# Kernel tuning notes

Measured on AMD Instinct MI355X. Metric: run time of the kernel, lower is better.

## Reference

```python
import jax, jax.numpy as jnp
import numpy as np

N, H, W, C, CK, ITER = 4, 256, 256, 8, 2, 4
HID = 2 * C
C2 = C * C


def project(x, w1, b1, w2, b2, w3, b3):
    # flax Project: Dense->gelu->Dense->gelu->Dense (gelu approximate=tanh, jax default)
    h = jax.nn.gelu(x @ w1 + b1)
    h = jax.nn.gelu(h @ w2 + b2)
    return h @ w3 + b3


def setup_inputs() -> dict:
    key = jax.random.key(0)
    ks = jax.random.split(key, 40)
    d = {}
    d['u'] = jax.random.normal(ks[0], (N, H, W, C), jnp.float32)
    d['k'] = jax.random.normal(ks[1], (N, H, W, CK), jnp.float32)
    idx = 2
    # gamma MLP (in CK), delta MLP (in CK), greens real/imag MLPs (in 2)
    for nm, fin in zip(['g', 'dl', 'fr', 'fi'], [CK, CK, 2, 2]):
        for li, (fi_, fo) in enumerate([(fin, HID), (HID, HID), (HID, C2)]):
            d[f'{nm}_w{li+1}'] = jax.random.normal(ks[idx], (fi_, fo), jnp.float32) / np.sqrt(fi_).astype(np.float32)
            d[f'{nm}_b{li+1}'] = jnp.zeros((fo,), jnp.float32)
            idx += 1
    d['bias'] = jax.random.normal(ks[idx], (C,), jnp.float32)
    return d


def reference(u, k, g_w1, g_b1, g_w2, g_b2, g_w3, g_b3,
              dl_w1, dl_b1, dl_w2, dl_b2, dl_w3, dl_b3,
              fr_w1, fr_b1, fr_w2, fr_b2, fr_w3, fr_b3,
              fi_w1, fi_b1, fi_w2, fi_b2, fi_w3, fi_b3, bias):
    # per-pixel gamma / delta matrices: (N,H,W,C,C), scaled by 1/C^2 as in original
    gmat = (project(k, g_w1, g_b1, g_w2, g_b2, g_w3, g_b3) / C2).reshape(N, H, W, C, C)
    dmat = (project(k, dl_w1, dl_b1, dl_w2, dl_b2, dl_w3, dl_b3) / C2).reshape(N, H, W, C, C)
    # spectral Green's filter on the rfft grid; meshgrid(kx, ky) -> (W, H//2+1)
    kx = jnp.fft.rfftfreq(H, d=1.0 / H)
    ky = jnp.fft.fftfreq(W, d=1.0 / W)
    Kx, Ky = jnp.meshgrid(kx, ky)
    K = jnp.stack([Kx, Ky], axis=-1).astype(jnp.float32)  # (W, H//2+1, 2)
    filt_r = project(K, fr_w1, fr_b1, fr_w2, fr_b2, fr_w3, fr_b3)
    filt_i = project(K, fi_w1, fi_b1, fi_w2, fi_b2, fi_w3, fi_b3)
    filt = ((filt_r + 1j * filt_i) / C2).reshape(W, H // 2 + 1, C, C)  # H==W
    for _ in range(ITER):
        local = 2.0 * u - jnp.einsum('nhwj,nhwjk->nhwk', u, gmat)
        du = jnp.einsum('nhwj,nhwjk->nhwk', u, dmat)
        uf = jnp.fft.rfftn(du, axes=(1, 2))  # (N,H,W//2+1,C) complex
        gu = jnp.fft.irfftn(jnp.einsum('nhwj,hwjk->nhwk', uf, filt), axes=(1, 2))
        u = local + jnp.einsum('nhwj,nhwjk->nhwk', gu, gmat)
    return jax.nn.gelu(u + bias)
```

## Files before the change

kernel.cpp:

```cpp
#include <hip/hip_runtime.h>
#include <math.h>

#define NB 4
#define HB 256
#define WB 256
#define CB 8
#define NPIX (NB*HB*WB)
#define W2B 129
#define TWO_PI_F 6.283185307179586f

typedef float f32x4 __attribute__((ext_vector_type(4)));

__device__ __forceinline__ float gelu_f(float x){
    float z = 0.7978845608028654f*(x + 0.044715f*x*x*x);
    return x * __builtin_amdgcn_rcpf(1.0f + __expf(-2.0f*z));
}

__device__ __forceinline__ unsigned pack_bf16x2(float a, float b){
    unsigned ua = __float_as_uint(a), ub = __float_as_uint(b);
    ua = (ua + 0x7FFFu + ((ua >> 16) & 1u)) >> 16;
    ub = (ub + 0x7FFFu + ((ub >> 16) & 1u)) >> 16;
    return ua | (ub << 16);
}
__device__ __forceinline__ float2 unpack_bf16x2(unsigned v){
    return make_float2(__uint_as_float(v << 16), __uint_as_float(v & 0xFFFF0000u));
}

__device__ __forceinline__ void ldcp(float* dst, const float* __restrict__ src, int n, int t){
    for (int i = t; i < n; i += 256) dst[i] = src[i];
}

__global__ __launch_bounds__(256) void prep_kernel(
    const float* __restrict__ kin,
    const float* gw1,const float* gb1,const float* gw2,const float* gb2,const float* gw3,const float* gb3,
    const float* dw1,const float* db1,const float* dw2,const float* db2,const float* dw3,const float* db3,
    const float* fw1,const float* fb1,const float* fw2,const float* fb2,const float* fw3,const float* fb3,
    const float* iw1,const float* ib1,const float* iw2,const float* ib2,const float* iw3,const float* ib3,
    unsigned* __restrict__ gmat, unsigned* __restrict__ dmat,
    unsigned* __restrict__ fpack)
{
    __shared__ __align__(16) float sw[2816];
    int t = threadIdx.x;
    int b = blockIdx.x;
    if (b >= 129){
        int gd = (b >= 641);
        const float* w1 = gd ? dw1 : gw1;  const float* b1 = gd ? db1 : gb1;
        const float* w2 = gd ? dw2 : gw2;  const float* b2 = gd ? db2 : gb2;
        const float* w3 = gd ? dw3 : gw3;  const float* b3 = gd ? db3 : gb3;
        ldcp(sw+0,   w1,  32, t); ldcp(sw+32,  b1, 16, t);
        ldcp(sw+48,  w2, 256, t); ldcp(sw+304, b2, 16, t);
        ldcp(sw+320, w3,1024, t); ldcp(sw+1344,b3, 64, t);
        __syncthreads();
        unsigned* mat = gd ? dmat : gmat;
        int p0 = (b - (gd ? 641 : 129))*512 + t;
        int p1 = p0 + 256;
        float2 kv0 = ((const float2*)kin)[p0];
        float2 kv1 = ((const float2*)kin)[p1];
        size_t base0 = (size_t)(p0 >> 6)*2048 + (size_t)(p0 & 63)*4;
        size_t base1 = (size_t)(p1 >> 6)*2048 + (size_t)(p1 & 63)*4;
        float h1[2][16], h2[2][16];
#pragma unroll
        for (int o = 0; o < 16; ++o){
            float wx = sw[o], wy = sw[16+o], bo = sw[32+o];
            h1[0][o] = gelu_f(kv0.x*wx + kv0.y*wy + bo);
            h1[1][o] = gelu_f(kv1.x*wx + kv1.y*wy + bo);
        }
#pragma unroll
        for (int oc = 0; oc < 4; ++oc){
            f32x4 bb = *(const f32x4*)(sw + 304 + oc*4);
            f32x4 a0 = bb, a1 = bb;
#pragma unroll
            for (int i = 0; i < 16; ++i){
                f32x4 w = *(const f32x4*)(sw + 48 + i*16 + oc*4);
                a0 += h1[0][i]*w; a1 += h1[1][i]*w;
            }
            h2[0][oc*4+0]=gelu_f(a0.x); h2[0][oc*4+1]=gelu_f(a0.y);
            h2[0][oc*4+2]=gelu_f(a0.z); h2[0][oc*4+3]=gelu_f(a0.w);
            h2[1][oc*4+0]=gelu_f(a1.x); h2[1][oc*4+1]=gelu_f(a1.y);
            h2[1][oc*4+2]=gelu_f(a1.z); h2[1][oc*4+3]=gelu_f(a1.w);
        }
        const float s = 1.0f/64.0f;
#pragma unroll
        for (int j = 0; j < 8; ++j){
            f32x4 bA = *(const f32x4*)(sw + 1344 + j*8);
            f32x4 bB = *(const f32x4*)(sw + 1344 + j*8 + 4);
            f32x4 A0 = bA, A1 = bB, B0 = bA, B1 = bB;
#pragma unroll
            for (int i = 0; i < 16; ++i){
                f32x4 wA = *(const f32x4*)(sw + 320 + i*64 + j*8);
                f32x4 wB = *(const f32x4*)(sw + 320 + i*64 + j*8 + 4);
                float h0 = h2[0][i], h1v = h2[1][i];
                A0 += h0*wA; A1 += h0*wB;
                B0 += h1v*wA; B1 += h1v*wB;
            }
            uint4 o0 = { pack_bf16x2(A0.x*s,A0.y*s), pack_bf16x2(A0.z*s,A0.w*s),
                         pack_bf16x2(A1.x*s,A1.y*s), pack_bf16x2(A1.z*s,A1.w*s) };
            uint4 o1 = { pack_bf16x2(B0.x*s,B0.y*s), pack_bf16x2(B0.z*s,B0.w*s),
                         pack_bf16x2(B1.x*s,B1.y*s), pack_bf16x2(B1.z*s,B1.w*s) };
            *(uint4*)(mat + base0 + (size_t)j*256) = o0;
            *(uint4*)(mat + base1 + (size_t)j*256) = o1;
        }
    } else {
        ldcp(sw+0,   fw1,  32, t); ldcp(sw+32,  fb1, 16, t);
        ldcp(sw+48,  fw2, 256, t); ldcp(sw+304, fb2, 16, t);
        ldcp(sw+320, fw3,1024, t); ldcp(sw+1344,fb3, 64, t);
        ldcp(sw+1408+0,   iw1,  32, t); ldcp(sw+1408+32,  ib1, 16, t);
        ldcp(sw+1408+48,  iw2, 256, t); ldcp(sw+1408+304, ib2, 16, t);
        ldcp(sw+1408+320, iw3,1024, t); ldcp(sw+1408+1344,ib3, 64, t);
        __syncthreads();
        int w2 = b;
        float x = (float)w2;
        float y = (float)(t < 128 ? t : t - 256);
        float h1r[16], h1i[16], h2r[16], h2i[16];
#pragma unroll
        for (int o = 0; o < 16; ++o){
            h1r[o] = gelu_f(x*sw[o] + y*sw[16+o] + sw[32+o]);
            h1i[o] = gelu_f(x*sw[1408+o] + y*sw[1408+16+o] + sw[1408+32+o]);
        }
#pragma unroll
        for (int o = 0; o < 16; ++o){
            float ar = sw[304+o], ai = sw[1408+304+o];
#pragma unroll
            for (int i = 0; i < 16; ++i){
                ar += h1r[i]*sw[48+i*16+o];
                ai += h1i[i]*sw[1408+48+i*16+o];
            }
            h2r[o] = gelu_f(ar); h2i[o] = gelu_f(ai);
        }
        const float s = 1.0f/64.0f;
#pragma unroll
        for (int q = 0; q < 16; ++q){
            f32x4 aR = *(const f32x4*)(sw + 1344 + q*4);
            f32x4 aI = *(const f32x4*)(sw + 1408 + 1344 + q*4);
#pragma unroll
            for (int i = 0; i < 16; ++i){
                aR += h2r[i] * *(const f32x4*)(sw + 320 + i*64 + q*4);
                aI += h2i[i] * *(const f32x4*)(sw + 1408 + 320 + i*64 + q*4);
            }
            uint4 out = { pack_bf16x2(aR.x*s, aI.x*s), pack_bf16x2(aR.y*s, aI.y*s),
                          pack_bf16x2(aR.z*s, aI.z*s), pack_bf16x2(aR.w*s, aI.w*s) };
            *(uint4*)(fpack + (size_t)w2*16384 + (size_t)q*1024 + (size_t)t*4) = out;
        }
    }
}

__device__ __forceinline__ void fft256v(f32x4* xr, f32x4* xi, int t, float sgn)
{
    int n2 = t >> 4, k1 = t & 15;
    float csA, snA; __sincosf(sgn*TWO_PI_F*(float)k1*(1.0f/16.0f), &snA, &csA);
    f32x4 ar = {0.f,0.f,0.f,0.f}, ai = {0.f,0.f,0.f,0.f};
    float cw = 1.f, sw = 0.f;
#pragma unroll
    for (int n1 = 0; n1 < 16; ++n1){
        f32x4 vr = xr[16*n1 + n2], vi = xi[16*n1 + n2];
        ar += vr*cw - vi*sw;
        ai += vr*sw + vi*cw;
        float cn = cw*csA - sw*snA;
        sw = cw*snA + sw*csA; cw = cn;
    }
    float cs2, sn2; __sincosf(sgn*TWO_PI_F*(float)(n2*k1)*(1.0f/256.0f), &sn2, &cs2);
    f32x4 br = ar*cs2 - ai*sn2;
    f32x4 bi = ar*sn2 + ai*cs2;
    __syncthreads();
    xr[t] = br; xi[t] = bi;
    __syncthreads();
    int k1b = t & 15, k2 = t >> 4;
    float csB, snB; __sincosf(sgn*TWO_PI_F*(float)k2*(1.0f/16.0f), &snB, &csB);
    f32x4 yr = {0.f,0.f,0.f,0.f}, yi = {0.f,0.f,0.f,0.f};
    cw = 1.f; sw = 0.f;
#pragma unroll
    for (int n2b = 0; n2b < 16; ++n2b){
        f32x4 br2 = xr[n2b*16 + k1b], bi2 = xi[n2b*16 + k1b];
        yr += br2*cw - bi2*sw;
        yi += br2*sw + bi2*cw;
        float cn = cw*csB - sw*snB;
        sw = cw*snB + sw*csB; cw = cn;
    }
    __syncthreads();
    xr[t] = yr; xi[t] = yi;
    __syncthreads();
}

__device__ __forceinline__ void fft256v_core(f32x4* xr, f32x4* xi, int t, float sgn,
                                             f32x4& outR, f32x4& outI)
{
    int n2 = t >> 4, k1 = t & 15;
    float csA, snA; __sincosf(sgn*TWO_PI_F*(float)k1*(1.0f/16.0f), &snA, &csA);
    f32x4 ar = {0.f,0.f,0.f,0.f}, ai = {0.f,0.f,0.f,0.f};
    float cw = 1.f, sw = 0.f;
#pragma unroll
    for (int n1 = 0; n1 < 16; ++n1){
        f32x4 vr = xr[16*n1 + n2], vi = xi[16*n1 + n2];
        ar += vr*cw - vi*sw;
        ai += vr*sw + vi*cw;
        float cn = cw*csA - sw*snA;
        sw = cw*snA + sw*csA; cw = cn;
    }
    float cs2, sn2; __sincosf(sgn*TWO_PI_F*(float)(n2*k1)*(1.0f/256.0f), &sn2, &cs2);
    f32x4 br = ar*cs2 - ai*sn2;
    f32x4 bi = ar*sn2 + ai*cs2;
    __syncthreads();
    xr[t] = br; xi[t] = bi;
    __syncthreads();
    int k1b = t & 15, k2 = t >> 4;
    float csB, snB; __sincosf(sgn*TWO_PI_F*(float)k2*(1.0f/16.0f), &snB, &csB);
    f32x4 yr = {0.f,0.f,0.f,0.f}, yi = {0.f,0.f,0.f,0.f};
    cw = 1.f; sw = 0.f;
#pragma unroll
    for (int n2b = 0; n2b < 16; ++n2b){
        f32x4 br2 = xr[n2b*16 + k1b], bi2 = xi[n2b*16 + k1b];
        yr += br2*cw - bi2*sw;
        yi += br2*sw + bi2*cw;
        float cn = cw*csB - sw*snB;
        sw = cw*snB + sw*csB; cw = cn;
    }
    outR = yr; outI = yi;
}

__device__ __forceinline__ void fft256v8_core(
    f32x4 (*xr)[256], f32x4 (*xi)[256], int t, float sgn,
    f32x4& o0R, f32x4& o0I, f32x4& o1R, f32x4& o1I)
{
    int n2 = t >> 4, k1 = t & 15;
    float csA, snA; __sincosf(sgn*TWO_PI_F*(float)k1*(1.0f/16.0f), &snA, &csA);
    f32x4 a0r={0.f,0.f,0.f,0.f}, a0i=a0r, a1r=a0r, a1i=a0r;
    float cw = 1.f, sw = 0.f;
#pragma unroll
    for (int n1 = 0; n1 < 16; ++n1){
        int idx = 16*n1 + n2;
        f32x4 v0r = xr[0][idx], v0i = xi[0][idx];
        f32x4 v1r = xr[1][idx], v1i = xi[1][idx];
        a0r += v0r*cw - v0i*sw;  a0i += v0r*sw + v0i*cw;
        a1r += v1r*cw - v1i*sw;  a1i += v1r*sw + v1i*cw;
        float cn = cw*csA - sw*snA;
        sw = cw*snA + sw*csA; cw = cn;
    }
    float cs2, sn2; __sincosf(sgn*TWO_PI_F*(float)(n2*k1)*(1.0f/256.0f), &sn2, &cs2);
    f32x4 b0r = a0r*cs2 - a0i*sn2, b0i = a0r*sn2 + a0i*cs2;
    f32x4 b1r = a1r*cs2 - a1i*sn2, b1i = a1r*sn2 + a1i*cs2;
    __syncthreads();
    xr[0][t]=b0r; xi[0][t]=b0i; xr[1][t]=b1r; xi[1][t]=b1i;
    __syncthreads();
    int k1b = t & 15, k2 = t >> 4;
    float csB, snB; __sincosf(sgn*TWO_PI_F*(float)k2*(1.0f/16.0f), &snB, &csB);
    f32x4 y0r={0.f,0.f,0.f,0.f}, y0i=y0r, y1r=y0r, y1i=y0r;
    cw = 1.f; sw = 0.f;
#pragma unroll
    for (int n2b = 0; n2b < 16; ++n2b){
        int idx = n2b*16 + k1b;
        f32x4 c0r = xr[0][idx], c0i = xi[0][idx];
        f32x4 c1r = xr[1][idx], c1i = xi[1][idx];
        y0r += c0r*cw - c0i*sw;  y0i += c0r*sw + c0i*cw;
        y1r += c1r*cw - c1i*sw;  y1i += c1r*sw + c1i*cw;
        float cn = cw*csB - sw*snB;
        sw = cw*snB + sw*csB; cw = cn;
    }
    o0R = y0r; o0I = y0i; o1R = y1r; o1I = y1i;
}

__device__ __forceinline__ void fwd_store(
    f32x4* XR, f32x4* XI, const float* dv, int t, int n, int h,
    float2* __restrict__ spec)
{
    XR[t] = (f32x4){dv[0],dv[2],dv[4],dv[6]};
    XI[t] = (f32x4){dv[1],dv[3],dv[5],dv[7]};
    __syncthreads();
    fft256v(XR, XI, t, -1.f);
    if (t <= 128){
        int m = (256 - t) & 255;
        f32x4 zr = XR[t], zi = XI[t], yr = XR[m], yi = XI[m];
        float4* dst = (float4*)(spec + (((size_t)n*129 + t)*256 + h)*8);
        dst[0] = make_float4(0.5f*(zr.x+yr.x), 0.5f*(zi.x-yi.x), 0.5f*(zi.x+yi.x), 0.5f*(yr.x-zr.x));
        dst[1] = make_float4(0.5f*(zr.y+yr.y), 0.5f*(zi.y-yi.y), 0.5f*(zi.y+yi.y), 0.5f*(yr.y-zr.y));
        dst[2] = make_float4(0.5f*(zr.z+yr.z), 0.5f*(zi.z-yi.z), 0.5f*(zi.z+yi.z), 0.5f*(yr.z-zr.z));
        dst[3] = make_float4(0.5f*(zr.w+yr.w), 0.5f*(zi.w-yi.w), 0.5f*(zi.w+yi.w), 0.5f*(yr.w-zr.w));
    }
}

__device__ __forceinline__ void inv_fft_to_gu(
    const float2* __restrict__ spec, f32x4* XR, f32x4* XI,
    int t, int n, int h, float* gu)
{
    int w2 = (t <= 128) ? t : 256 - t;
    const float4* rp = (const float4*)(spec + (((size_t)n*129 + w2)*256 + h)*8);
    float4 q0 = rp[0], q1 = rp[1], q2 = rp[2], q3 = rp[3];
    f32x4 xr, xi;
    if (t <= 128){
        xr = (f32x4){q0.x - q0.w, q1.x - q1.w, q2.x - q2.w, q3.x - q3.w};
        xi = (f32x4){q0.y + q0.z, q1.y + q1.z, q2.y + q2.z, q3.y + q3.z};
    } else {
        xr = (f32x4){ q0.x + q0.w,  q1.x + q1.w,  q2.x + q2.w,  q3.x + q3.w};
        xi = (f32x4){-q0.y + q0.z, -q1.y + q1.z, -q2.y + q2.z, -q3.y + q3.z};
    }
    XR[t] = xr; XI[t] = xi;
    __syncthreads();
    f32x4 gr, gi;
    fft256v_core(XR, XI, t, +1.f, gr, gi);
    const float s = 1.0f/65536.0f;
    gu[0]=gr.x*s; gu[1]=gi.x*s; gu[2]=gr.y*s; gu[3]=gi.y*s;
    gu[4]=gr.z*s; gu[5]=gi.z*s; gu[6]=gr.w*s; gu[7]=gi.w*s;
}

__device__ __forceinline__ void matvec_acc(const unsigned* __restrict__ mat,
                                           size_t base, const float* v, float* acc)
{
    const uint4* mp = (const uint4*)(mat + base);
#pragma unroll
    for (int j = 0; j < 8; ++j){
        uint4 q = mp[j*64];
        float vj = v[j];
        float2 f0 = unpack_bf16x2(q.x), f1 = unpack_bf16x2(q.y);
        float2 f2 = unpack_bf16x2(q.z), f3 = unpack_bf16x2(q.w);
        acc[0] += vj*f0.x; acc[1] += vj*f0.y;
        acc[2] += vj*f1.x; acc[3] += vj*f1.y;
        acc[4] += vj*f2.x; acc[5] += vj*f2.y;
        acc[6] += vj*f3.x; acc[7] += vj*f3.y;
    }
}

__global__ __launch_bounds__(256) void fft_fwd_kernel(
    const float* __restrict__ u, const unsigned* __restrict__ dmat,
    float2* __restrict__ spec)
{
    __shared__ f32x4 XR[256], XI[256];
    int t = threadIdx.x, bid = blockIdx.x;
    int n = bid >> 8, h = bid & 255;
    const float* up = u + (size_t)bid*2048 + (size_t)t*8;
    float4 ua = ((const float4*)up)[0], ub = ((const float4*)up)[1];
    float uv[8] = {ua.x,ua.y,ua.z,ua.w, ub.x,ub.y,ub.z,ub.w};
    size_t base = (size_t)(bid*4 + (t>>6))*2048 + (size_t)(t&63)*4;
    float dv[8] = {0,0,0,0,0,0,0,0};
    matvec_acc(dmat, base, uv, dv);
    fwd_store(XR, XI, dv, t, n, h, spec);
}

__global__ __launch_bounds__(256) void ffth_mult_kernel(
    float2* __restrict__ spec, const unsigned* __restrict__ fpack)
{
    __shared__ f32x4 XR[2][256], XI[2][256];
    int t = threadIdx.x;
    int n = blockIdx.x / 129, w2 = blockIdx.x % 129;
    float2* base = spec + ((size_t)(n*129 + w2))*2048;
    const float4* rp = (const float4*)(base + (size_t)t*8);
    float4 r0 = rp[0], r1 = rp[1], r2 = rp[2], r3 = rp[3];
    XR[0][t] = (f32x4){r0.x, r0.z, r1.x, r1.z};
    XI[0][t] = (f32x4){r0.y, r0.w, r1.y, r1.w};
    XR[1][t] = (f32x4){r2.x, r2.z, r3.x, r3.z};
    XI[1][t] = (f32x4){r2.y, r2.w, r3.y, r3.w};
    __syncthreads();
    f32x4 s0R, s0I, s1R, s1I;
    fft256v8_core(XR, XI, t, -1.f, s0R, s0I, s1R, s1I);

    float sr[8] = {s0R.x,s0R.y,s0R.z,s0R.w, s1R.x,s1R.y,s1R.z,s1R.w};
    float si[8] = {s0I.x,s0I.y,s0I.z,s0I.w, s1I.x,s1I.y,s1I.z,s1I.w};
    f32x4 o0R={0.f,0.f,0.f,0.f}, o0I=o0R, o1R=o0R, o1I=o0R;
    const uint4* fp = (const uint4*)(fpack + (size_t)w2*16384 + (size_t)t*4);
#pragma unroll
    for (int j = 0; j < 8; ++j){
        float sjr = sr[j], sji = si[j];
        uint4 fa = fp[(j*2+0)*256];
        uint4 fb = fp[(j*2+1)*256];
        float2 f0 = unpack_bf16x2(fa.x), f1 = unpack_bf16x2(fa.y);
        float2 f2 = unpack_bf16x2(fa.z), f3 = unpack_bf16x2(fa.w);
        o0R.x += sjr*f0.x - sji*f0.y;  o0I.x += sjr*f0.y + sji*f0.x;
        o0R.y += sjr*f1.x - sji*f1.y;  o0I.y += sjr*f1.y + sji*f1.x;
        o0R.z += sjr*f2.x - sji*f2.y;  o0I.z += sjr*f2.y + sji*f2.x;
        o0R.w += sjr*f3.x - sji*f3.y;  o0I.w += sjr*f3.y + sji*f3.x;
        float2 g0 = unpack_bf16x2(fb.x), g1 = unpack_bf16x2(fb.y);
        float2 g2 = unpack_bf16x2(fb.z), g3 = unpack_bf16x2(fb.w);
        o1R.x += sjr*g0.x - sji*g0.y;  o1I.x += sjr*g0.y + sji*g0.x;
        o1R.y += sjr*g1.x - sji*g1.y;  o1I.y += sjr*g1.y + sji*g1.x;
        o1R.z += sjr*g2.x - sji*g2.y;  o1I.z += sjr*g2.y + sji*g2.x;
        o1R.w += sjr*g3.x - sji*g3.y;  o1I.w += sjr*g3.y + sji*g3.x;
    }
    __syncthreads();
    XR[0][t]=o0R; XI[0][t]=o0I; XR[1][t]=o1R; XI[1][t]=o1I;
    __syncthreads();
    f32x4 v0R, v0I, v1R, v1I;
    fft256v8_core(XR, XI, t, +1.f, v0R, v0I, v1R, v1I);
    float4* wp = (float4*)(base + (size_t)t*8);
    wp[0] = make_float4(v0R.x, v0I.x, v0R.y, v0I.y);
    wp[1] = make_float4(v0R.z, v0I.z, v0R.w, v0I.w);
    wp[2] = make_float4(v1R.x, v1I.x, v1R.y, v1I.y);
    wp[3] = make_float4(v1R.z, v1I.z, v1R.w, v1I.w);
}

__global__ __launch_bounds__(256) void born_step_kernel(
    float2* __restrict__ spec, const float* __restrict__ u_in,
    float* __restrict__ u_out, const unsigned* __restrict__ gmat,
    const unsigned* __restrict__ dmat)
{
    __shared__ f32x4 XR[256], XI[256];
    int t = threadIdx.x, bid = blockIdx.x;
    int n = bid >> 8, h = bid & 255;
    float gu[8];
    inv_fft_to_gu(spec, XR, XI, t, n, h, gu);

    const float* up = u_in + (size_t)bid*2048 + (size_t)t*8;
    float4 ua = ((const float4*)up)[0], ub = ((const float4*)up)[1];
    float uv[8] = {ua.x,ua.y,ua.z,ua.w, ub.x,ub.y,ub.z,ub.w};
    float e[8], acc[8];
#pragma unroll
    for (int c = 0; c < 8; ++c){ e[c] = gu[c] - uv[c]; acc[c] = 2.0f*uv[c]; }
    size_t base = (size_t)(bid*4 + (t>>6))*2048 + (size_t)(t&63)*4;
    matvec_acc(gmat, base, e, acc);
    float* op = u_out + (size_t)bid*2048 + (size_t)t*8;
    ((float4*)op)[0] = make_float4(acc[0],acc[1],acc[2],acc[3]);
    ((float4*)op)[1] = make_float4(acc[4],acc[5],acc[6],acc[7]);

    float dv[8] = {0,0,0,0,0,0,0,0};
    matvec_acc(dmat, base, acc, dv);
    __syncthreads();
    fwd_store(XR, XI, dv, t, n, h, spec);
}

__global__ __launch_bounds__(256) void final_kernel(
    const float2* __restrict__ spec, const float* __restrict__ u_in,
    const unsigned* __restrict__ gmat, const float* __restrict__ bias,
    float* __restrict__ out)
{
    __shared__ f32x4 XR[256], XI[256];
    int t = threadIdx.x, bid = blockIdx.x;
    int n = bid >> 8, h = bid & 255;
    float gu[8];
    inv_fft_to_gu(spec, XR, XI, t, n, h, gu);

    const float* up = u_in + (size_t)bid*2048 + (size_t)t*8;
    float4 ua = ((const float4*)up)[0], ub = ((const float4*)up)[1];
    float uv[8] = {ua.x,ua.y,ua.z,ua.w, ub.x,ub.y,ub.z,ub.w};
    float e[8], acc[8];
#pragma unroll
    for (int c = 0; c < 8; ++c){ e[c] = gu[c] - uv[c]; acc[c] = 2.0f*uv[c]; }
    size_t base = (size_t)(bid*4 + (t>>6))*2048 + (size_t)(t&63)*4;
    matvec_acc(gmat, base, e, acc);
#pragma unroll
    for (int k = 0; k < 8; ++k) acc[k] = gelu_f(acc[k] + bias[k]);
    float* op = out + (size_t)bid*2048 + (size_t)t*8;
    ((float4*)op)[0] = make_float4(acc[0],acc[1],acc[2],acc[3]);
    ((float4*)op)[1] = make_float4(acc[4],acc[5],acc[6],acc[7]);
}

extern "C" void kernel_launch(void* const* d_in, const int* in_sizes, int n_in,
                              void* d_out, int out_size, void* d_ws, size_t ws_size,
                              hipStream_t stream) {
    const float* u_in = (const float*)d_in[0];
    const float* k_in = (const float*)d_in[1];
    const float* Wp[24];
    for (int i = 0; i < 24; ++i) Wp[i] = (const float*)d_in[2+i];
    const float* bias = (const float*)d_in[26];

    char* base = (char*)d_ws;
    unsigned* gmat  = (unsigned*)(base);
    unsigned* dmat  = (unsigned*)(base + 33554432ull);
    unsigned* fpack = (unsigned*)(base + 67108864ull);
    float*    u_ws  = (float*)   (base + 75563008ull);
    float2*   spec  = (float2*)  (base + 83951616ull);

    prep_kernel<<<1153, 256, 0, stream>>>(k_in,
        Wp[0],Wp[1],Wp[2],Wp[3],Wp[4],Wp[5],
        Wp[6],Wp[7],Wp[8],Wp[9],Wp[10],Wp[11],
        Wp[12],Wp[13],Wp[14],Wp[15],Wp[16],Wp[17],
        Wp[18],Wp[19],Wp[20],Wp[21],Wp[22],Wp[23],
        gmat, dmat, fpack);

    fft_fwd_kernel<<<1024, 256, 0, stream>>>(u_in, dmat, spec);
    for (int it = 0; it < 4; ++it){
        ffth_mult_kernel<<<516, 256, 0, stream>>>(spec, fpack);
        if (it < 3){
            born_step_kernel<<<1024, 256, 0, stream>>>(
                spec, (it == 0) ? u_in : u_ws, u_ws, gmat, dmat);
        } else {
            final_kernel<<<1024, 256, 0, stream>>>(spec, u_ws, gmat, bias, (float*)d_out);
        }
    }
}
```

Before: 211.0 us.

## Process two rows per block in row FFT kernels using batched FFT core

The forward FFT, Born-step and final kernels now handle two image rows per block instead of one. They use the existing two-row fft256v8_core, which shares twiddle computation and barriers across both rows, and the grid shrinks from 1024 to 512 blocks. The aim is to amortize sincos and synchronization overhead and raise instruction-level parallelism. In exchange, each block uses twice the shared memory and more registers, and with fewer blocks on a 256-CU device occupancy and latency hiding may drop.

```diff
diff --git a/kernel.cpp b/kernel.cpp
--- a/kernel.cpp
+++ b/kernel.cpp
@@ -144,79 +144,6 @@
     }
 }
 
-__device__ __forceinline__ void fft256v(f32x4* xr, f32x4* xi, int t, float sgn)
-{
-    int n2 = t >> 4, k1 = t & 15;
-    float csA, snA; __sincosf(sgn*TWO_PI_F*(float)k1*(1.0f/16.0f), &snA, &csA);
-    f32x4 ar = {0.f,0.f,0.f,0.f}, ai = {0.f,0.f,0.f,0.f};
-    float cw = 1.f, sw = 0.f;
-#pragma unroll
-    for (int n1 = 0; n1 < 16; ++n1){
-        f32x4 vr = xr[16*n1 + n2], vi = xi[16*n1 + n2];
-        ar += vr*cw - vi*sw;
-        ai += vr*sw + vi*cw;
-        float cn = cw*csA - sw*snA;
-        sw = cw*snA + sw*csA; cw = cn;
-    }
-    float cs2, sn2; __sincosf(sgn*TWO_PI_F*(float)(n2*k1)*(1.0f/256.0f), &sn2, &cs2);
-    f32x4 br = ar*cs2 - ai*sn2;
-    f32x4 bi = ar*sn2 + ai*cs2;
-    __syncthreads();
-    xr[t] = br; xi[t] = bi;
-    __syncthreads();
-    int k1b = t & 15, k2 = t >> 4;
-    float csB, snB; __sincosf(sgn*TWO_PI_F*(float)k2*(1.0f/16.0f), &snB, &csB);
-    f32x4 yr = {0.f,0.f,0.f,0.f}, yi = {0.f,0.f,0.f,0.f};
-    cw = 1.f; sw = 0.f;
-#pragma unroll
-    for (int n2b = 0; n2b < 16; ++n2b){
-        f32x4 br2 = xr[n2b*16 + k1b], bi2 = xi[n2b*16 + k1b];
-        yr += br2*cw - bi2*sw;
-        yi += br2*sw + bi2*cw;
-        float cn = cw*csB - sw*snB;
-        sw = cw*snB + sw*csB; cw = cn;
-    }
-    __syncthreads();
-    xr[t] = yr; xi[t] = yi;
-    __syncthreads();
-}
-
-__device__ __forceinline__ void fft256v_core(f32x4* xr, f32x4* xi, int t, float sgn,
-                                             f32x4& outR, f32x4& outI)
-{
-    int n2 = t >> 4, k1 = t & 15;
-    float csA, snA; __sincosf(sgn*TWO_PI_F*(float)k1*(1.0f/16.0f), &snA, &csA);
-    f32x4 ar = {0.f,0.f,0.f,0.f}, ai = {0.f,0.f,0.f,0.f};
-    float cw = 1.f, sw = 0.f;
-#pragma unroll
-    for (int n1 = 0; n1 < 16; ++n1){
-        f32x4 vr = xr[16*n1 + n2], vi = xi[16*n1 + n2];
-        ar += vr*cw - vi*sw;
-        ai += vr*sw + vi*cw;
-        float cn = cw*csA - sw*snA;
-        sw = cw*snA + sw*csA; cw = cn;
-    }
-    float cs2, sn2; __sincosf(sgn*TWO_PI_F*(float)(n2*k1)*(1.0f/256.0f), &sn2, &cs2);
-    f32x4 br = ar*cs2 - ai*sn2;
-    f32x4 bi = ar*sn2 + ai*cs2;
-    __syncthreads();
-    xr[t] = br; xi[t] = bi;
-    __syncthreads();
-    int k1b = t & 15, k2 = t >> 4;
-    float csB, snB; __sincosf(sgn*TWO_PI_F*(float)k2*(1.0f/16.0f), &snB, &csB);
-    f32x4 yr = {0.f,0.f,0.f,0.f}, yi = {0.f,0.f,0.f,0.f};
-    cw = 1.f; sw = 0.f;
-#pragma unroll
-    for (int n2b = 0; n2b < 16; ++n2b){
-        f32x4 br2 = xr[n2b*16 + k1b], bi2 = xi[n2b*16 + k1b];
-        yr += br2*cw - bi2*sw;
-        yi += br2*sw + bi2*cw;
-        float cn = cw*csB - sw*snB;
-        sw = cw*snB + sw*csB; cw = cn;
-    }
-    outR = yr; outI = yi;
-}
-
 __device__ __forceinline__ void fft256v8_core(
     f32x4 (*xr)[256], f32x4 (*xi)[256], int t, float sgn,
     f32x4& o0R, f32x4& o0I, f32x4& o1R, f32x4& o1I)
@@ -258,33 +185,38 @@
     o0R = y0r; o0I = y0i; o1R = y1r; o1I = y1i;
 }
 
-__device__ __forceinline__ void fwd_store(
-    f32x4* XR, f32x4* XI, const float* dv, int t, int n, int h,
-    float2* __restrict__ spec)
-{
-    XR[t] = (f32x4){dv[0],dv[2],dv[4],dv[6]};
-    XI[t] = (f32x4){dv[1],dv[3],dv[5],dv[7]};
-    __syncthreads();
-    fft256v(XR, XI, t, -1.f);
+__device__ __forceinline__ void fwd_store2(
+    f32x4 (*XR)[256], f32x4 (*XI)[256], const float* dv0, const float* dv1,
+    int t, int n, int h0, float2* __restrict__ spec)
+{
+    XR[0][t] = (f32x4){dv0[0],dv0[2],dv0[4],dv0[6]};
+    XI[0][t] = (f32x4){dv0[1],dv0[3],dv0[5],dv0[7]};
+    XR[1][t] = (f32x4){dv1[0],dv1[2],dv1[4],dv1[6]};
+    XI[1][t] = (f32x4){dv1[1],dv1[3],dv1[5],dv1[7]};
+    __syncthreads();
+    f32x4 y0R, y0I, y1R, y1I;
+    fft256v8_core(XR, XI, t, -1.f, y0R, y0I, y1R, y1I);
+    __syncthreads();
+    XR[0][t]=y0R; XI[0][t]=y0I; XR[1][t]=y1R; XI[1][t]=y1I;
+    __syncthreads();
     if (t <= 128){
         int m = (256 - t) & 255;
-        f32x4 zr = XR[t], zi = XI[t], yr = XR[m], yi = XI[m];
-        float4* dst = (float4*)(spec + (((size_t)n*129 + t)*256 + h)*8);
-        dst[0] = make_float4(0.5f*(zr.x+yr.x), 0.5f*(zi.x-yi.x), 0.5f*(zi.x+yi.x), 0.5f*(yr.x-zr.x));
-        dst[1] = make_float4(0.5f*(zr.y+yr.y), 0.5f*(zi.y-yi.y), 0.5f*(zi.y+yi.y), 0.5f*(yr.y-zr.y));
-        dst[2] = make_float4(0.5f*(zr.z+yr.z), 0.5f*(zi.z-yi.z), 0.5f*(zi.z+yi.z), 0.5f*(yr.z-zr.z));
-        dst[3] = make_float4(0.5f*(zr.w+yr.w), 0.5f*(zi.w-yi.w), 0.5f*(zi.w+yi.w), 0.5f*(yr.w-zr.w));
-    }
-}
-
-__device__ __forceinline__ void inv_fft_to_gu(
-    const float2* __restrict__ spec, f32x4* XR, f32x4* XI,
-    int t, int n, int h, float* gu)
-{
-    int w2 = (t <= 128) ? t : 256 - t;
-    const float4* rp = (const float4*)(spec + (((size_t)n*129 + w2)*256 + h)*8);
-    float4 q0 = rp[0], q1 = rp[1], q2 = rp[2], q3 = rp[3];
-    f32x4 xr, xi;
+#pragma unroll
+        for (int r = 0; r < 2; ++r){
+            f32x4 zr = XR[r][t], zi = XI[r][t], yr = XR[r][m], yi = XI[r][m];
+            float4* dst = (float4*)(spec + (((size_t)n*129 + t)*256 + (h0+r))*8);
+            dst[0] = make_float4(0.5f*(zr.x+yr.x), 0.5f*(zi.x-yi.x), 0.5f*(zi.x+yi.x), 0.5f*(yr.x-zr.x));
+            dst[1] = make_float4(0.5f*(zr.y+yr.y), 0.5f*(zi.y-yi.y), 0.5f*(zi.y+yi.y), 0.5f*(yr.y-zr.y));
+            dst[2] = make_float4(0.5f*(zr.z+yr.z), 0.5f*(zi.z-yi.z), 0.5f*(zi.z+yi.z), 0.5f*(yr.z-zr.z));
+            dst[3] = make_float4(0.5f*(zr.w+yr.w), 0.5f*(zi.w-yi.w), 0.5f*(zi.w+yi.w), 0.5f*(yr.w-zr.w));
+        }
+    }
+}
+
+__device__ __forceinline__ void herm_pack(
+    const float4& q0, const float4& q1, const float4& q2, const float4& q3,
+    int t, f32x4& xr, f32x4& xi)
+{
     if (t <= 128){
         xr = (f32x4){q0.x - q0.w, q1.x - q1.w, q2.x - q2.w, q3.x - q3.w};
         xi = (f32x4){q0.y + q0.z, q1.y + q1.z, q2.y + q2.z, q3.y + q3.z};
@@ -292,13 +224,28 @@
         xr = (f32x4){ q0.x + q0.w,  q1.x + q1.w,  q2.x + q2.w,  q3.x + q3.w};
         xi = (f32x4){-q0.y + q0.z, -q1.y + q1.z, -q2.y + q2.z, -q3.y + q3.z};
     }
-    XR[t] = xr; XI[t] = xi;
-    __syncthreads();
-    f32x4 gr, gi;
-    fft256v_core(XR, XI, t, +1.f, gr, gi);
+}
+
+__device__ __forceinline__ void inv_fft_to_gu2(
+    const float2* __restrict__ spec, f32x4 (*XR)[256], f32x4 (*XI)[256],
+    int t, int n, int h0, float* gu0, float* gu1)
+{
+    int w2 = (t <= 128) ? t : 256 - t;
+    const float4* rp0 = (const float4*)(spec + (((size_t)n*129 + w2)*256 + h0)*8);
+    const float4* rp1 = (const float4*)(spec + (((size_t)n*129 + w2)*256 + h0+1)*8);
+    float4 a0=rp0[0], a1=rp0[1], a2=rp0[2], a3=rp0[3];
+    float4 b0=rp1[0], b1=rp1[1], b2=rp1[2], b3=rp1[3];
+    f32x4 xr, xi;
+    herm_pack(a0,a1,a2,a3, t, xr, xi);  XR[0][t]=xr; XI[0][t]=xi;
+    herm_pack(b0,b1,b2,b3, t, xr, xi);  XR[1][t]=xr; XI[1][t]=xi;
+    __syncthreads();
+    f32x4 g0r,g0i,g1r,g1i;
+    fft256v8_core(XR, XI, t, +1.f, g0r,g0i,g1r,g1i);
     const float s = 1.0f/65536.0f;
-    gu[0]=gr.x*s; gu[1]=gi.x*s; gu[2]=gr.y*s; gu[3]=gi.y*s;
-    gu[4]=gr.z*s; gu[5]=gi.z*s; gu[6]=gr.w*s; gu[7]=gi.w*s;
+    gu0[0]=g0r.x*s; gu0[1]=g0i.x*s; gu0[2]=g0r.y*s; gu0[3]=g0i.y*s;
+    gu0[4]=g0r.z*s; gu0[5]=g0i.z*s; gu0[6]=g0r.w*s; gu0[7]=g0i.w*s;
+    gu1[0]=g1r.x*s; gu1[1]=g1i.x*s; gu1[2]=g1r.y*s; gu1[3]=g1i.y*s;
+    gu1[4]=g1r.z*s; gu1[5]=g1i.z*s; gu1[6]=g1r.w*s; gu1[7]=g1i.w*s;
 }
 
 __device__ __forceinline__ void matvec_acc(const unsigned* __restrict__ mat,
@@ -318,20 +265,31 @@
     }
 }
 
+__device__ __forceinline__ void load8(const float* p, float* v){
+    float4 a = ((const float4*)p)[0], b = ((const float4*)p)[1];
+    v[0]=a.x; v[1]=a.y; v[2]=a.z; v[3]=a.w; v[4]=b.x; v[5]=b.y; v[6]=b.z; v[7]=b.w;
+}
+__device__ __forceinline__ void store8(float* p, const float* v){
+    ((float4*)p)[0] = make_float4(v[0],v[1],v[2],v[3]);
+    ((float4*)p)[1] = make_float4(v[4],v[5],v[6],v[7]);
+}
+
 __global__ __launch_bounds__(256) void fft_fwd_kernel(
     const float* __restrict__ u, const unsigned* __restrict__ dmat,
     float2* __restrict__ spec)
 {
-    __shared__ f32x4 XR[256], XI[256];
+    __shared__ f32x4 XR[2][256], XI[2][256];
     int t = threadIdx.x, bid = blockIdx.x;
-    int n = bid >> 8, h = bid & 255;
-    const float* up = u + (size_t)bid*2048 + (size_t)t*8;
-    float4 ua = ((const float4*)up)[0], ub = ((const float4*)up)[1];
-    float uv[8] = {ua.x,ua.y,ua.z,ua.w, ub.x,ub.y,ub.z,ub.w};
-    size_t base = (size_t)(bid*4 + (t>>6))*2048 + (size_t)(t&63)*4;
-    float dv[8] = {0,0,0,0,0,0,0,0};
-    matvec_acc(dmat, base, uv, dv);
-    fwd_store(XR, XI, dv, t, n, h, spec);
+    int n = bid >> 7, h0 = (bid & 127)*2;
+    float uv0[8], uv1[8], dv0[8]={0,0,0,0,0,0,0,0}, dv1[8]={0,0,0,0,0,0,0,0};
+    size_t row0 = (size_t)(n*256 + h0);
+    load8(u + row0*2048 + (size_t)t*8, uv0);
+    load8(u + (row0+1)*2048 + (size_t)t*8, uv1);
+    size_t base0 = (row0*4 + (t>>6))*2048 + (size_t)(t&63)*4;
+    size_t base1 = ((row0+1)*4 + (t>>6))*2048 + (size_t)(t&63)*4;
+    matvec_acc(dmat, base0, uv0, dv0);
+    matvec_acc(dmat, base1, uv1, dv1);
+    fwd_store2(XR, XI, dv0, dv1, t, n, h0, spec);
 }
 
 __global__ __launch_bounds__(256) void ffth_mult_kernel(
@@ -390,28 +348,35 @@
     float* __restrict__ u_out, const unsigned* __restrict__ gmat,
     const unsigned* __restrict__ dmat)
 {
-    __shared__ f32x4 XR[256], XI[256];
+    __shared__ f32x4 XR[2][256], XI[2][256];
     int t = threadIdx.x, bid = blockIdx.x;
-    int n = bid >> 8, h = bid & 255;
-    float gu[8];
-    inv_fft_to_gu(spec, XR, XI, t, n, h, gu);
-
-    const float* up = u_in + (size_t)bid*2048 + (size_t)t*8;
-    float4 ua = ((const float4*)up)[0], ub = ((const float4*)up)[1];
-    float uv[8] = {ua.x,ua.y,ua.z,ua.w, ub.x,ub.y,ub.z,ub.w};
-    float e[8], acc[8];
-#pragma unroll
-    for (int c = 0; c < 8; ++c){ e[c] = gu[c] - uv[c]; acc[c] = 2.0f*uv[c]; }
-    size_t base = (size_t)(bid*4 + (t>>6))*2048 + (size_t)(t&63)*4;
-    matvec_acc(gmat, base, e, acc);
-    float* op = u_out + (size_t)bid*2048 + (size_t)t*8;
-    ((float4*)op)[0] = make_float4(acc[0],acc[1],acc[2],acc[3]);
-    ((float4*)op)[1] = make_float4(acc[4],acc[5],acc[6],acc[7]);
-
-    float dv[8] = {0,0,0,0,0,0,0,0};
-    matvec_acc(dmat, base, acc, dv);
-    __syncthreads();
-    fwd_store(XR, XI, dv, t, n, h, spec);
+    int n = bid >> 7, h0 = (bid & 127)*2;
+    float gu0[8], gu1[8];
+    inv_fft_to_gu2(spec, XR, XI, t, n, h0, gu0, gu1);
+
+    size_t row0 = (size_t)(n*256 + h0);
+    float uv0[8], uv1[8];
+    load8(u_in + row0*2048 + (size_t)t*8, uv0);
+    load8(u_in + (row0+1)*2048 + (size_t)t*8, uv1);
+    size_t base0 = (row0*4 + (t>>6))*2048 + (size_t)(t&63)*4;
+    size_t base1 = ((row0+1)*4 + (t>>6))*2048 + (size_t)(t&63)*4;
+
+    float e0[8], acc0[8], e1[8], acc1[8];
+#pragma unroll
+    for (int c = 0; c < 8; ++c){
+        e0[c] = gu0[c] - uv0[c]; acc0[c] = 2.0f*uv0[c];
+        e1[c] = gu1[c] - uv1[c]; acc1[c] = 2.0f*uv1[c];
+    }
+    matvec_acc(gmat, base0, e0, acc0);
+    matvec_acc(gmat, base1, e1, acc1);
+    store8(u_out + row0*2048 + (size_t)t*8, acc0);
+    store8(u_out + (row0+1)*2048 + (size_t)t*8, acc1);
+
+    float dv0[8]={0,0,0,0,0,0,0,0}, dv1[8]={0,0,0,0,0,0,0,0};
+    matvec_acc(dmat, base0, acc0, dv0);
+    matvec_acc(dmat, base1, acc1, dv1);
+    __syncthreads();
+    fwd_store2(XR, XI, dv0, dv1, t, n, h0, spec);
 }
 
 __global__ __launch_bounds__(256) void final_kernel(
@@ -419,25 +384,34 @@
     const unsigned* __restrict__ gmat, const float* __restrict__ bias,
     float* __restrict__ out)
 {
-    __shared__ f32x4 XR[256], XI[256];
+    __shared__ f32x4 XR[2][256], XI[2][256];
     int t = threadIdx.x, bid = blockIdx.x;
-    int n = bid >> 8, h = bid & 255;
-    float gu[8];
-    inv_fft_to_gu(spec, XR, XI, t, n, h, gu);
-
-    const float* up = u_in + (size_t)bid*2048 + (size_t)t*8;
-    float4 ua = ((const float4*)up)[0], ub = ((const float4*)up)[1];
-    float uv[8] = {ua.x,ua.y,ua.z,ua.w, ub.x,ub.y,ub.z,ub.w};
-    float e[8], acc[8];
-#pragma unroll
-    for (int c = 0; c < 8; ++c){ e[c] = gu[c] - uv[c]; acc[c] = 2.0f*uv[c]; }
-    size_t base = (size_t)(bid*4 + (t>>6))*2048 + (size_t)(t&63)*4;
-    matvec_acc(gmat, base, e, acc);
-#pragma unroll
-    for (int k = 0; k < 8; ++k) acc[k] = gelu_f(acc[k] + bias[k]);
-    float* op = out + (size_t)bid*2048 + (size_t)t*8;
-    ((float4*)op)[0] = make_float4(acc[0],acc[1],acc[2],acc[3]);
-    ((float4*)op)[1] = make_float4(acc[4],acc[5],acc[6],acc[7]);
+    int n = bid >> 7, h0 = (bid & 127)*2;
+    float gu0[8], gu1[8];
+    inv_fft_to_gu2(spec, XR, XI, t, n, h0, gu0, gu1);
+
+    size_t row0 = (size_t)(n*256 + h0);
+    float uv0[8], uv1[8];
+    load8(u_in + row0*2048 + (size_t)t*8, uv0);
+    load8(u_in + (row0+1)*2048 + (size_t)t*8, uv1);
+    size_t base0 = (row0*4 + (t>>6))*2048 + (size_t)(t&63)*4;
+    size_t base1 = ((row0+1)*4 + (t>>6))*2048 + (size_t)(t&63)*4;
+
+    float e0[8], acc0[8], e1[8], acc1[8];
+#pragma unroll
+    for (int c = 0; c < 8; ++c){
+        e0[c] = gu0[c] - uv0[c]; acc0[c] = 2.0f*uv0[c];
+        e1[c] = gu1[c] - uv1[c]; acc1[c] = 2.0f*uv1[c];
+    }
+    matvec_acc(gmat, base0, e0, acc0);
+    matvec_acc(gmat, base1, e1, acc1);
+#pragma unroll
+    for (int k = 0; k < 8; ++k){
+        acc0[k] = gelu_f(acc0[k] + bias[k]);
+        acc1[k] = gelu_f(acc1[k] + bias[k]);
+    }
+    store8(out + row0*2048 + (size_t)t*8, acc0);
+    store8(out + (row0+1)*2048 + (size_t)t*8, acc1);
 }
 
 extern "C" void kernel_launch(void* const* d_in, const int* in_sizes, int n_in,
@@ -463,14 +437,14 @@
         Wp[18],Wp[19],Wp[20],Wp[21],Wp[22],Wp[23],
         gmat, dmat, fpack);
 
-    fft_fwd_kernel<<<1024, 256, 0, stream>>>(u_in, dmat, spec);
+    fft_fwd_kernel<<<512, 256, 0, stream>>>(u_in, dmat, spec);
     for (int it = 0; it < 4; ++it){
         ffth_mult_kernel<<<516, 256, 0, stream>>>(spec, fpack);
         if (it < 3){
-            born_step_kernel<<<1024, 256, 0, stream>>>(
+            born_step_kernel<<<512, 256, 0, stream>>>(
                 spec, (it == 0) ? u_in : u_ws, u_ws, gmat, dmat);
         } else {
-            final_kernel<<<1024, 256, 0, stream>>>(spec, u_ws, gmat, bias, (float*)d_out);
-        }
-    }
-}
+            final_kernel<<<512, 256, 0, stream>>>(spec, u_ws, gmat, bias, (float*)d_out);
+        }
+    }
+}
```

Result: no change. 214.7 us (+1.8%).
